# Kernel optimization log

Measured on AMD Instinct MI355X. Metric: run time of the kernel, lower is better.

The kernel has to match this reference:

```python
import jax, jax.numpy as jnp
import numpy as np

N_NODES = 50000
N_EDGES = 800000
IN_F = 256
HID = 128
OUT_F = 128
HEADS = 4
NEG_SLOPE = 0.2


def setup_inputs() -> dict:
    key = jax.random.key(0)
    ks = jax.random.split(key, 10)
    x = jax.random.normal(ks[0], (N_NODES, IN_F), dtype=jnp.float32)
    edge_index = jax.random.randint(ks[1], (2, N_EDGES), 0, N_NODES, dtype=jnp.int64)
    # layer 1: in=256 -> heads=4, ch=128
    W1 = jax.random.normal(ks[2], (HEADS * HID, IN_F), dtype=jnp.float32) / np.sqrt(IN_F)
    att_src1 = jax.random.normal(ks[3], (HEADS, HID), dtype=jnp.float32) / np.sqrt(HID)
    att_dst1 = jax.random.normal(ks[4], (HEADS, HID), dtype=jnp.float32) / np.sqrt(HID)
    b1 = jnp.zeros((HID,), dtype=jnp.float32)
    # layer 2: in=128 -> heads=4, ch=128
    W2 = jax.random.normal(ks[5], (HEADS * OUT_F, HID), dtype=jnp.float32) / np.sqrt(HID)
    att_src2 = jax.random.normal(ks[6], (HEADS, OUT_F), dtype=jnp.float32) / np.sqrt(OUT_F)
    att_dst2 = jax.random.normal(ks[7], (HEADS, OUT_F), dtype=jnp.float32) / np.sqrt(OUT_F)
    b2 = jnp.zeros((OUT_F,), dtype=jnp.float32)
    return {"x": x, "edge_index": edge_index,
            "W1": W1, "att_src1": att_src1, "att_dst1": att_dst1, "b1": b1,
            "W2": W2, "att_src2": att_src2, "att_dst2": att_dst2, "b2": b2}


def gat_conv(x, src, dst, W, att_src, att_dst, b, heads, ch):
    n = x.shape[0]
    xh = (x @ W.T).reshape(n, heads, ch)                 # [N,H,C]
    a_s = jnp.einsum('nhc,hc->nh', xh, att_src)          # [N,H]
    a_d = jnp.einsum('nhc,hc->nh', xh, att_dst)
    alpha = a_s[src] + a_d[dst]                          # [E,H]
    alpha = jnp.where(alpha >= 0, alpha, NEG_SLOPE * alpha)
    # segment softmax over destination nodes
    amax = jax.ops.segment_max(alpha, dst, num_segments=n)
    amax = jnp.where(jnp.isfinite(amax), amax, 0.0)
    e = jnp.exp(alpha - amax[dst])                       # [E,H]
    denom = jax.ops.segment_sum(e, dst, num_segments=n)  # [N,H]
    coef = e / (denom[dst] + 1e-16)                      # [E,H]
    msg = xh[src] * coef[:, :, None]                     # [E,H,C]
    out = jax.ops.segment_sum(msg, dst, num_segments=n)  # [N,H,C]
    return out.mean(axis=1) + b                          # concat=False -> mean over heads


def reference(x, edge_index, W1, att_src1, att_dst1, b1, W2, att_src2, att_dst2, b2):
    n = x.shape[0]
    loops = jnp.arange(n, dtype=edge_index.dtype)
    src = jnp.concatenate([edge_index[0], loops])        # add_self_loops=True (PyG default)
    dst = jnp.concatenate([edge_index[1], loops])
    h = gat_conv(x, src, dst, W1, att_src1, att_dst1, b1, HEADS, HID)
    return gat_conv(h, src, dst, W2, att_src2, att_dst2, b2, HEADS, OUT_F)
```

## Files before the change

### kernel.cpp

```cpp
#include <hip/hip_runtime.h>
#include <hip/hip_fp16.h>
#include <math.h>

#define N_NODES 50000
#define MPAD    50176
#define N_EDGES 800000
#define E_TOT   (N_EDGES + N_NODES)
#define EB      ((E_TOT + 255) / 256)
#define HEADS   4
#define NEG_SLOPE 0.2f
#define SBLK    ((N_NODES + 255) / 256)

typedef unsigned int u32;
typedef unsigned short u16;
typedef __attribute__((ext_vector_type(8))) _Float16 f16x8;
typedef __attribute__((ext_vector_type(4))) float f32x4;



__global__ __launch_bounds__(256) void prep(const int* __restrict__ ei,
                                            int* __restrict__ deg,
                                            int* __restrict__ epos,
                                            const float* __restrict__ W1,
                                            __half* __restrict__ B1,
                                            const float* __restrict__ W2,
                                            __half* __restrict__ B2,
                                            const float* __restrict__ att_s1,
                                            const float* __restrict__ att_d1,
                                            const float* __restrict__ att_s2,
                                            const float* __restrict__ att_d2,
                                            float* __restrict__ ws1,
                                            float* __restrict__ wd1,
                                            float* __restrict__ ws2,
                                            float* __restrict__ wd2) {
  int b = blockIdx.x, tid = threadIdx.x;
  if (b < EB) {
    int e = b * 256 + tid;
    if (e < E_TOT) {
      int dst = (e < N_EDGES) ? ei[N_EDGES + e] : (e - N_EDGES);
      epos[e] = atomicAdd(&deg[dst], 1);
    }
    return;
  }
  if (b < EB + 128) {
    int k4 = (b - EB) * 256 + tid;
    float4 v = ((const float4*)W1)[k4];
    __half2 h01 = __float22half2_rn(make_float2(v.x, v.y));
    __half2 h23 = __float22half2_rn(make_float2(v.z, v.w));
    uint2 pk = make_uint2(*(u32*)&h01, *(u32*)&h23);
    int r = k4 >> 6, h = r >> 7, j = r & 127;
    ((uint2*)B1)[j * 256 + h * 64 + (k4 & 63)] = pk;
    return;
  }
  if (b < EB + 192) {
    int k4 = (b - EB - 128) * 256 + tid;
    float4 v = ((const float4*)W2)[k4];
    __half2 h01 = __float22half2_rn(make_float2(v.x, v.y));
    __half2 h23 = __float22half2_rn(make_float2(v.z, v.w));
    uint2 pk = make_uint2(*(u32*)&h01, *(u32*)&h23);
    int r = k4 >> 5, h = r >> 7, j = r & 127;
    ((uint2*)B2)[j * 128 + h * 32 + (k4 & 31)] = pk;
    return;
  }
  int bw = b - (EB + 192);
  int h = bw & 3;
  if (bw < 8) {
    const float* att = (bw < 4) ? att_s1 : att_d1;
    float* o = (bw < 4) ? ws1 : wd1;
    int k = tid;
    float acc = 0.f;
    for (int c = 0; c < 128; ++c)
      acc = fmaf(att[h * 128 + c], W1[(size_t)(h * 128 + c) * 256 + k], acc);
    o[h * 256 + k] = acc;
  } else {
    const float* att = (bw < 12) ? att_s2 : att_d2;
    float* o = (bw < 12) ? ws2 : wd2;
    if (tid < 128) {
      int k = tid;
      float acc = 0.f;
      for (int c = 0; c < 128; ++c)
        acc = fmaf(att[h * 128 + c], W2[(size_t)(h * 128 + c) * 128 + k], acc);
      o[h * 128 + k] = acc;
    }
  }
}


__global__ __launch_bounds__(256) void scan_blocks(const int* __restrict__ deg,
                                                   int* __restrict__ row_ptr,
                                                   int* __restrict__ bsum) {
  __shared__ int sh[256];
  int tid = threadIdx.x;
  int idx = blockIdx.x * 256 + tid;
  int v = (idx < N_NODES) ? deg[idx] : 0;
  sh[tid] = v;
  __syncthreads();
#pragma unroll
  for (int off = 1; off < 256; off <<= 1) {
    int t = (tid >= off) ? sh[tid - off] : 0;
    __syncthreads();
    sh[tid] += t;
    __syncthreads();
  }
  if (idx < N_NODES) row_ptr[idx + 1] = sh[tid];
  if (tid == 255) bsum[blockIdx.x] = sh[255];
}

__global__ __launch_bounds__(256) void scan_tops(int* __restrict__ bsum) {
  __shared__ int sh[256];
  int tid = threadIdx.x;
  int v = (tid < SBLK) ? bsum[tid] : 0;
  sh[tid] = v;
  __syncthreads();
#pragma unroll
  for (int off = 1; off < 256; off <<= 1) {
    int t = (tid >= off) ? sh[tid - off] : 0;
    __syncthreads();
    sh[tid] += t;
    __syncthreads();
  }
  if (tid < SBLK) bsum[tid] = sh[tid] - v;
}

__global__ __launch_bounds__(256) void scan_add(const int* __restrict__ bsum,
                                                int* __restrict__ row_ptr) {
  int idx = blockIdx.x * 256 + threadIdx.x;
  int off = bsum[blockIdx.x];
  if (idx < N_NODES) row_ptr[idx + 1] += off;
  if (idx == 0) row_ptr[0] = 0;
}

__device__ __forceinline__ float leaky_exp(float a) {
  a = (a >= 0.f) ? a : NEG_SLOPE * a;
  return __expf(a);
}


__global__ __launch_bounds__(256) void scatter_pos(const int* __restrict__ ei,
                                                   const int* __restrict__ epos,
                                                   const int* __restrict__ row_ptr,
                                                   int2* __restrict__ col2) {
  int e = blockIdx.x * 256 + threadIdx.x;
  if (e >= E_TOT) return;
  int src, dst;
  if (e < N_EDGES) { src = ei[e]; dst = ei[N_EDGES + e]; }
  else             { src = e - N_EDGES; dst = src; }
  int slot = row_ptr[dst] + epos[e];
  col2[slot] = make_int2(src, dst);
}


__global__ __launch_bounds__(256) void edge_weights(const int2* __restrict__ col2,
                                                    const float* __restrict__ as_,
                                                    const float* __restrict__ ad_,
                                                    float4* __restrict__ wtab) {
  int i = blockIdx.x * 256 + threadIdx.x;
  if (i >= E_TOT) return;
  int2 sd = col2[i];
  float4 a = ((const float4*)as_)[sd.x];
  float4 d = ((const float4*)ad_)[sd.y];
  float4 w;
  w.x = leaky_exp(a.x + d.x);
  w.y = leaky_exp(a.y + d.y);
  w.z = leaky_exp(a.z + d.z);
  w.w = leaky_exp(a.w + d.w);
  wtab[i] = w;
}


__global__ __launch_bounds__(256) void prep_x(const float* __restrict__ x,
                                              const float* __restrict__ ws1,
                                              const float* __restrict__ wd1,
                                              __half* __restrict__ x16,
                                              float* __restrict__ as_,
                                              float* __restrict__ ad_) {
  int node = (blockIdx.x * 256 + threadIdx.x) >> 6;
  if (node >= N_NODES) return;
  int lane = threadIdx.x & 63;
  int c4 = lane * 4;
  f32x4 xv = *(const f32x4*)(x + (size_t)node * 256 + c4);
  __half2 h01 = __float22half2_rn(make_float2(xv[0], xv[1]));
  __half2 h23 = __float22half2_rn(make_float2(xv[2], xv[3]));
  uint2 pk = make_uint2(*(u32*)&h01, *(u32*)&h23);
  *(uint2*)(x16 + (size_t)node * 256 + c4) = pk;
  float p[8];
#pragma unroll
  for (int v = 0; v < 4; ++v) {
    f32x4 w = *(const f32x4*)(ws1 + v * 256 + c4);
    p[v] = xv[0] * w[0] + xv[1] * w[1] + xv[2] * w[2] + xv[3] * w[3];
    f32x4 u = *(const f32x4*)(wd1 + v * 256 + c4);
    p[4 + v] = xv[0] * u[0] + xv[1] * u[1] + xv[2] * u[2] + xv[3] * u[3];
  }
#pragma unroll
  for (int k = 0; k < 8; ++k)
#pragma unroll
    for (int m = 1; m < 64; m <<= 1)
      p[k] += __shfl_xor(p[k], m, 64);
  if (lane == 0) {
    *(float4*)(as_ + (size_t)node * 4) = make_float4(p[0], p[1], p[2], p[3]);
    *(float4*)(ad_ + (size_t)node * 4) = make_float4(p[4], p[5], p[6], p[7]);
  }
}


__global__ __launch_bounds__(256) void score2(const __half* __restrict__ hrow,
                                              const float* __restrict__ ws2,
                                              const float* __restrict__ wd2,
                                              float* __restrict__ as_,
                                              float* __restrict__ ad_) {
  int node = (blockIdx.x * 256 + threadIdx.x) >> 6;
  if (node >= N_NODES) return;
  int lane = threadIdx.x & 63, c = lane * 2;
  float2 f = __half22float2(*(const __half2*)(hrow + (size_t)node * 128 + c));
  float p[8];
#pragma unroll
  for (int v = 0; v < 4; ++v) {
    float2 w = *(const float2*)(ws2 + v * 128 + c);
    p[v] = f.x * w.x + f.y * w.y;
    float2 u = *(const float2*)(wd2 + v * 128 + c);
    p[4 + v] = f.x * u.x + f.y * u.y;
  }
#pragma unroll
  for (int k = 0; k < 8; ++k)
#pragma unroll
    for (int m = 1; m < 64; m <<= 1)
      p[k] += __shfl_xor(p[k], m, 64);
  if (lane == 0) {
    *(float4*)(as_ + (size_t)node * 4) = make_float4(p[0], p[1], p[2], p[3]);
    *(float4*)(ad_ + (size_t)node * 4) = make_float4(p[4], p[5], p[6], p[7]);
  }
}


template <int CPL>
__global__ __launch_bounds__(256) void gat_aggregate_w(
    const __half* __restrict__ tbl, const float4* __restrict__ wtab,
    const int* __restrict__ row_ptr, const int2* __restrict__ col2,
    __half* __restrict__ agg) {
  constexpr int CHIN = CPL * 64;
  const int* colx = (const int*)col2;
  int node = (blockIdx.x * 256 + threadIdx.x) >> 6;
  if (node >= N_NODES) return;
  int lane = threadIdx.x & 63, cb = lane * CPL;
  const __half* tb = tbl + cb;
  int s = __builtin_amdgcn_readfirstlane(row_ptr[node]);
  int e = __builtin_amdgcn_readfirstlane(row_ptr[node + 1]);

  float acc[4][CPL];
#pragma unroll
  for (int h = 0; h < 4; ++h)
#pragma unroll
    for (int c = 0; c < CPL; ++c) acc[h][c] = 0.f;
  float den[4] = {0.f, 0.f, 0.f, 0.f};

  auto accum = [&](uint2 q, float4 w) {
    float wv[4] = {w.x, w.y, w.z, w.w};
#pragma unroll
    for (int h = 0; h < 4; ++h) den[h] += wv[h];
    float f[CPL];
    float2 f0 = __half22float2(*(__half2*)&q.x);
    f[0] = f0.x; f[1] = f0.y;
    if (CPL == 4) {
      float2 f1 = __half22float2(*(__half2*)&q.y);
      f[2] = f1.x; f[3] = f1.y;
    }
#pragma unroll
    for (int h = 0; h < 4; ++h)
#pragma unroll
      for (int c = 0; c < CPL; ++c)
        acc[h][c] = fmaf(wv[h], f[c], acc[h][c]);
  };
  auto loadq = [&](int src) -> uint2 {
    if (CPL == 4) return *(const uint2*)(tb + (size_t)src * CHIN);
    uint2 r; r.x = *(const u32*)(tb + (size_t)src * CHIN); r.y = 0;
    return r;
  };

  int i = s;
  for (; i + 4 <= e; i += 4) {
    int s0 = __builtin_amdgcn_readfirstlane(colx[2 * i]);
    int s1 = __builtin_amdgcn_readfirstlane(colx[2 * i + 2]);
    int s2 = __builtin_amdgcn_readfirstlane(colx[2 * i + 4]);
    int s3 = __builtin_amdgcn_readfirstlane(colx[2 * i + 6]);
    float4 w0 = wtab[i],     w1 = wtab[i + 1];
    float4 w2 = wtab[i + 2], w3 = wtab[i + 3];
    uint2 q0 = loadq(s0), q1 = loadq(s1), q2 = loadq(s2), q3 = loadq(s3);
    accum(q0, w0); accum(q1, w1); accum(q2, w2); accum(q3, w3);
  }
  for (; i < e; ++i) {
    int s0 = __builtin_amdgcn_readfirstlane(colx[2 * i]);
    float4 w0 = wtab[i];
    accum(loadq(s0), w0);
  }

#pragma unroll
  for (int h = 0; h < 4; ++h) {
    float inv = 1.f / (den[h] + 1e-16f);
    if (CPL == 4) {
      __half2 o0 = __float22half2_rn(make_float2(acc[h][0] * inv, acc[h][1] * inv));
      __half2 o1 = __float22half2_rn(make_float2(acc[h][2] * inv, acc[h][3] * inv));
      *(uint2*)(agg + (size_t)node * 4 * CHIN + h * CHIN + cb) =
          make_uint2(*(u32*)&o0, *(u32*)&o1);
    } else {
      __half2 o0 = __float22half2_rn(make_float2(acc[h][0] * inv, acc[h][1] * inv));
      *(u32*)(agg + (size_t)node * 4 * CHIN + h * CHIN + cb) = *(u32*)&o0;
    }
  }
}


#define GLD16(gp, lp)                                                          \
  __builtin_amdgcn_global_load_lds(                                            \
      (const __attribute__((address_space(1))) u32*)(gp),                      \
      (__attribute__((address_space(3))) u32*)(lp), 16, 0, 0)

template <int K, bool HALF_OUT>
__global__ __launch_bounds__(512, 4) void gemm_mean(
    const __half* __restrict__ A, const __half* __restrict__ Bm,
    const float* __restrict__ bias, void* __restrict__ outv) {
  __shared__ u16 sA[256 * 32];
  __shared__ u16 sB[128 * 32];
  const int tid = threadIdx.x, lane = tid & 63, wave = tid >> 6;
  const int m0 = blockIdx.x * 256;
  const int wm = (wave >> 1) * 64, wn = (wave & 1) * 64;
  const int t = lane & 15, quad = lane >> 4;

  f32x4 acc[4][4];
#pragma unroll
  for (int i = 0; i < 4; i++)
#pragma unroll
    for (int j = 0; j < 4; j++) acc[i][j] = (f32x4){0.f, 0.f, 0.f, 0.f};

  const char* gpA[2]; u32 offA[2];
#pragma unroll
  for (int r = 0; r < 2; ++r) {
    int c = tid + r * 512;
    int row = c >> 2, w16 = c & 3;
    gpA[r] = (const char*)A + ((size_t)(m0 + row) * K) * 2 + w16 * 16;
    offA[r] = (u32)c * 16;
  }
  const char* gpB;
  {
    int row = tid >> 2, w16 = tid & 3;
    gpB = (const char*)Bm + ((size_t)row * K) * 2 + w16 * 16;
  }
  u32 offB = (u32)tid * 16;

  for (int k0 = 0; k0 < K; k0 += 32) {
    __syncthreads();
#pragma unroll
    for (int r = 0; r < 2; ++r) { GLD16(gpA[r], (char*)sA + offA[r]); gpA[r] += 64; }
    GLD16(gpB, (char*)sB + offB); gpB += 64;
    __syncthreads();

    f16x8 a[4], b[4];
#pragma unroll
    for (int i = 0; i < 4; ++i) {
      a[i] = *(const f16x8*)&sA[(wm + t + i * 16) * 32 + quad * 8];
      b[i] = *(const f16x8*)&sB[(wn + t + i * 16) * 32 + quad * 8];
    }
#pragma unroll
    for (int i = 0; i < 4; ++i)
#pragma unroll
      for (int j = 0; j < 4; ++j)
        acc[i][j] = __builtin_amdgcn_mfma_f32_16x16x32_f16(a[i], b[j], acc[i][j], 0, 0, 0);
  }

  float bv[4];
#pragma unroll
  for (int j = 0; j < 4; ++j) bv[j] = bias[wn + j * 16 + t];
#pragma unroll
  for (int i = 0; i < 4; ++i)
#pragma unroll
    for (int j = 0; j < 4; ++j)
#pragma unroll
      for (int r = 0; r < 4; ++r) {
        int m = m0 + wm + i * 16 + quad * 4 + r;
        if (m < N_NODES) {
          int n = wn + j * 16 + t;
          float v = 0.25f * acc[i][j][r] + bv[j];
          if (HALF_OUT) ((__half*)outv)[(size_t)m * 128 + n] = __float2half(v);
          else          ((float*)outv)[(size_t)m * 128 + n] = v;
        }
      }
}


extern "C" void kernel_launch(void* const* d_in, const int* in_sizes, int n_in,
                              void* d_out, int out_size, void* d_ws, size_t ws_size,
                              hipStream_t stream) {
  const float* x      = (const float*)d_in[0];
  const int*   ei     = (const int*)  d_in[1];
  const float* W1     = (const float*)d_in[2];
  const float* att_s1 = (const float*)d_in[3];
  const float* att_d1 = (const float*)d_in[4];
  const float* b1     = (const float*)d_in[5];
  const float* W2     = (const float*)d_in[6];
  const float* att_s2 = (const float*)d_in[7];
  const float* att_d2 = (const float*)d_in[8];
  const float* b2     = (const float*)d_in[9];
  float* out = (float*)d_out;

  char* ws = (char*)d_ws;
  size_t off = 0;
  auto alloc = [&](size_t bytes) -> void* {
    void* p = ws + off;
    off += (bytes + 255) & ~(size_t)255;
    return p;
  };
  __half* x16  = (__half*)alloc((size_t)MPAD * 256 * 2);
  __half* agg1 = (__half*)alloc((size_t)MPAD * 1024 * 2);
  __half* B1p  = (__half*)alloc((size_t)128 * 1024 * 2);
  __half* B2p  = (__half*)alloc((size_t)128 * 512 * 2);
  float* ws1 = (float*)alloc(4 * 256 * 4);
  float* wd1 = (float*)alloc(4 * 256 * 4);
  float* ws2 = (float*)alloc(4 * 128 * 4);
  float* wd2 = (float*)alloc(4 * 128 * 4);
  float* as1 = (float*)alloc((size_t)N_NODES * 4 * 4);
  float* ad1 = (float*)alloc((size_t)N_NODES * 4 * 4);
  float* as2 = (float*)alloc((size_t)N_NODES * 4 * 4);
  float* ad2 = (float*)alloc((size_t)N_NODES * 4 * 4);
  int*   row_ptr = (int*)alloc((size_t)(N_NODES + 1) * 4);
  int*   deg     = (int*)alloc((size_t)N_NODES * 4);
  int*   bsum    = (int*)alloc((size_t)256 * 4);
  int*   epos    = (int*)alloc((size_t)E_TOT * 4);
  int2*  col2    = (int2*)alloc((size_t)E_TOT * 8);
  float4* wtab   = (float4*)alloc((size_t)E_TOT * 16);

  __half* out1 = x16;
  __half* agg2 = agg1;

  const int edge_blocks = (E_TOT + 255) / 256;
  const int node_wave_blocks = (N_NODES + 3) / 4;

  hipMemsetAsync(deg, 0, (size_t)N_NODES * 4, stream);
  prep<<<EB + 208, 256, 0, stream>>>(ei, deg, epos, W1, B1p, W2, B2p,
                                     att_s1, att_d1, att_s2, att_d2,
                                     ws1, wd1, ws2, wd2);
  scan_blocks<<<SBLK, 256, 0, stream>>>(deg, row_ptr, bsum);
  scan_tops<<<1, 256, 0, stream>>>(bsum);
  scan_add<<<SBLK, 256, 0, stream>>>(bsum, row_ptr);
  scatter_pos<<<edge_blocks, 256, 0, stream>>>(ei, epos, row_ptr, col2);

  prep_x<<<node_wave_blocks, 256, 0, stream>>>(x, ws1, wd1, x16, as1, ad1);
  edge_weights<<<edge_blocks, 256, 0, stream>>>(col2, as1, ad1, wtab);
  gat_aggregate_w<4><<<node_wave_blocks, 256, 0, stream>>>(
      x16, wtab, row_ptr, col2, agg1);
  gemm_mean<1024, true><<<MPAD / 256, 512, 0, stream>>>(agg1, B1p, b1, out1);

  score2<<<node_wave_blocks, 256, 0, stream>>>(out1, ws2, wd2, as2, ad2);
  edge_weights<<<edge_blocks, 256, 0, stream>>>(col2, as2, ad2, wtab);
  gat_aggregate_w<2><<<node_wave_blocks, 256, 0, stream>>>(
      out1, wtab, row_ptr, col2, agg2);
  gemm_mean<512, false><<<MPAD / 256, 512, 0, stream>>>(agg2, B2p, b2, out);
}
```

Before: 406.6 us.

## Fuse neighbor aggregation with head-mean projection GEMM via shared memory

Each block now aggregates 16 destination nodes (4 per wave) into an LDS tile of weighted per-head features, then does the projection with MFMA straight from LDS and writes the biased head-mean output. This removes the large intermediate agg buffer (N×1024 halves for layer 1) and its global write and read, plus the separate GEMM launches. In exchange, B is reloaded from global/L2 by every block, each wave handles several nodes one after another, and the GEMM tile is small (16 rows), so MFMA efficiency and load balance may drop.

```diff
diff --git a/kernel.cpp b/kernel.cpp
--- a/kernel.cpp
+++ b/kernel.cpp
@@ -3,13 +3,13 @@
 #include <math.h>
 
 #define N_NODES 50000
-#define MPAD    50176
 #define N_EDGES 800000
 #define E_TOT   (N_EDGES + N_NODES)
 #define EB      ((E_TOT + 255) / 256)
 #define HEADS   4
 #define NEG_SLOPE 0.2f
 #define SBLK    ((N_NODES + 255) / 256)
+#define FBLK    (N_NODES / 16)
 
 typedef unsigned int u32;
 typedef unsigned short u16;
@@ -232,157 +232,120 @@
 }
 
 
-template <int CPL>
-__global__ __launch_bounds__(256) void gat_aggregate_w(
+template <int CPL, bool HALF_OUT>
+__global__ __launch_bounds__(256) void gat_fused(
     const __half* __restrict__ tbl, const float4* __restrict__ wtab,
     const int* __restrict__ row_ptr, const int2* __restrict__ col2,
-    __half* __restrict__ agg) {
+    const __half* __restrict__ Bm, const float* __restrict__ bias,
+    void* __restrict__ outv) {
   constexpr int CHIN = CPL * 64;
+  constexpr int K = 4 * CHIN;
+  constexpr int RST = K + 8;
+  __shared__ u16 sA[16 * RST];
+  const int tid = threadIdx.x, lane = tid & 63, wave = tid >> 6;
+  const int base = blockIdx.x * 16;
+  const int cb = lane * CPL;
+  const __half* tb = tbl + cb;
   const int* colx = (const int*)col2;
-  int node = (blockIdx.x * 256 + threadIdx.x) >> 6;
-  if (node >= N_NODES) return;
-  int lane = threadIdx.x & 63, cb = lane * CPL;
-  const __half* tb = tbl + cb;
-  int s = __builtin_amdgcn_readfirstlane(row_ptr[node]);
-  int e = __builtin_amdgcn_readfirstlane(row_ptr[node + 1]);
-
-  float acc[4][CPL];
-#pragma unroll
-  for (int h = 0; h < 4; ++h)
-#pragma unroll
-    for (int c = 0; c < CPL; ++c) acc[h][c] = 0.f;
-  float den[4] = {0.f, 0.f, 0.f, 0.f};
-
-  auto accum = [&](uint2 q, float4 w) {
-    float wv[4] = {w.x, w.y, w.z, w.w};
-#pragma unroll
-    for (int h = 0; h < 4; ++h) den[h] += wv[h];
-    float f[CPL];
-    float2 f0 = __half22float2(*(__half2*)&q.x);
-    f[0] = f0.x; f[1] = f0.y;
-    if (CPL == 4) {
-      float2 f1 = __half22float2(*(__half2*)&q.y);
-      f[2] = f1.x; f[3] = f1.y;
-    }
+
+  for (int nn = 0; nn < 4; ++nn) {
+    const int row = wave * 4 + nn;
+    const int node = base + row;
+    int s = __builtin_amdgcn_readfirstlane(row_ptr[node]);
+    int e = __builtin_amdgcn_readfirstlane(row_ptr[node + 1]);
+
+    float acc[4][CPL];
 #pragma unroll
     for (int h = 0; h < 4; ++h)
 #pragma unroll
-      for (int c = 0; c < CPL; ++c)
-        acc[h][c] = fmaf(wv[h], f[c], acc[h][c]);
-  };
-  auto loadq = [&](int src) -> uint2 {
-    if (CPL == 4) return *(const uint2*)(tb + (size_t)src * CHIN);
-    uint2 r; r.x = *(const u32*)(tb + (size_t)src * CHIN); r.y = 0;
-    return r;
-  };
-
-  int i = s;
-  for (; i + 4 <= e; i += 4) {
-    int s0 = __builtin_amdgcn_readfirstlane(colx[2 * i]);
-    int s1 = __builtin_amdgcn_readfirstlane(colx[2 * i + 2]);
-    int s2 = __builtin_amdgcn_readfirstlane(colx[2 * i + 4]);
-    int s3 = __builtin_amdgcn_readfirstlane(colx[2 * i + 6]);
-    float4 w0 = wtab[i],     w1 = wtab[i + 1];
-    float4 w2 = wtab[i + 2], w3 = wtab[i + 3];
-    uint2 q0 = loadq(s0), q1 = loadq(s1), q2 = loadq(s2), q3 = loadq(s3);
-    accum(q0, w0); accum(q1, w1); accum(q2, w2); accum(q3, w3);
-  }
-  for (; i < e; ++i) {
-    int s0 = __builtin_amdgcn_readfirstlane(colx[2 * i]);
-    float4 w0 = wtab[i];
-    accum(loadq(s0), w0);
-  }
-
-#pragma unroll
-  for (int h = 0; h < 4; ++h) {
-    float inv = 1.f / (den[h] + 1e-16f);
-    if (CPL == 4) {
-      __half2 o0 = __float22half2_rn(make_float2(acc[h][0] * inv, acc[h][1] * inv));
-      __half2 o1 = __float22half2_rn(make_float2(acc[h][2] * inv, acc[h][3] * inv));
-      *(uint2*)(agg + (size_t)node * 4 * CHIN + h * CHIN + cb) =
-          make_uint2(*(u32*)&o0, *(u32*)&o1);
+      for (int c = 0; c < CPL; ++c) acc[h][c] = 0.f;
+    float den[4] = {0.f, 0.f, 0.f, 0.f};
+
+    auto accum = [&](uint2 q, float4 w) {
+      float wv[4] = {w.x, w.y, w.z, w.w};
+#pragma unroll
+      for (int h = 0; h < 4; ++h) den[h] += wv[h];
+      float f[CPL];
+      float2 f0 = __half22float2(*(__half2*)&q.x);
+      f[0] = f0.x; f[1] = f0.y;
+      if (CPL == 4) {
+        float2 f1 = __half22float2(*(__half2*)&q.y);
+        f[2] = f1.x; f[3] = f1.y;
+      }
+#pragma unroll
+      for (int h = 0; h < 4; ++h)
+#pragma unroll
+        for (int c = 0; c < CPL; ++c)
+          acc[h][c] = fmaf(wv[h], f[c], acc[h][c]);
+    };
+    auto loadq = [&](int src) -> uint2 {
+      if (CPL == 4) return *(const uint2*)(tb + (size_t)src * CHIN);
+      uint2 r; r.x = *(const u32*)(tb + (size_t)src * CHIN); r.y = 0;
+      return r;
+    };
+
+    int i = s;
+    for (; i + 4 <= e; i += 4) {
+      int s0 = __builtin_amdgcn_readfirstlane(colx[2 * i]);
+      int s1 = __builtin_amdgcn_readfirstlane(colx[2 * i + 2]);
+      int s2 = __builtin_amdgcn_readfirstlane(colx[2 * i + 4]);
+      int s3 = __builtin_amdgcn_readfirstlane(colx[2 * i + 6]);
+      float4 w0 = wtab[i],     w1 = wtab[i + 1];
+      float4 w2 = wtab[i + 2], w3 = wtab[i + 3];
+      uint2 q0 = loadq(s0), q1 = loadq(s1), q2 = loadq(s2), q3 = loadq(s3);
+      accum(q0, w0); accum(q1, w1); accum(q2, w2); accum(q3, w3);
+    }
+    for (; i < e; ++i) {
+      int s0 = __builtin_amdgcn_readfirstlane(colx[2 * i]);
+      float4 w0 = wtab[i];
+      accum(loadq(s0), w0);
+    }
+
+#pragma unroll
+    for (int h = 0; h < 4; ++h) {
+      float inv = 1.f / (den[h] + 1e-16f);
+      if (CPL == 4) {
+        __half2 o0 = __float22half2_rn(make_float2(acc[h][0] * inv, acc[h][1] * inv));
+        __half2 o1 = __float22half2_rn(make_float2(acc[h][2] * inv, acc[h][3] * inv));
+        *(uint2*)&sA[row * RST + h * CHIN + cb] = make_uint2(*(u32*)&o0, *(u32*)&o1);
+      } else {
+        __half2 o0 = __float22half2_rn(make_float2(acc[h][0] * inv, acc[h][1] * inv));
+        *(u32*)&sA[row * RST + h * CHIN + cb] = *(u32*)&o0;
+      }
+    }
+  }
+  __syncthreads();
+
+  const int t = lane & 15, quad = lane >> 4;
+  f32x4 acc0 = (f32x4){0.f, 0.f, 0.f, 0.f};
+  f32x4 acc1 = (f32x4){0.f, 0.f, 0.f, 0.f};
+  const char* gB0 = (const char*)Bm + ((size_t)(wave * 32 + t) * K + quad * 8) * 2;
+  const char* gB1 = gB0 + (size_t)16 * K * 2;
+#pragma unroll 4
+  for (int k0 = 0; k0 < K; k0 += 32) {
+    f16x8 b0 = *(const f16x8*)(gB0 + (size_t)k0 * 2);
+    f16x8 b1 = *(const f16x8*)(gB1 + (size_t)k0 * 2);
+    f16x8 a = *(const f16x8*)&sA[t * RST + k0 + quad * 8];
+    acc0 = __builtin_amdgcn_mfma_f32_16x16x32_f16(a, b0, acc0, 0, 0, 0);
+    acc1 = __builtin_amdgcn_mfma_f32_16x16x32_f16(a, b1, acc1, 0, 0, 0);
+  }
+
+  const int n0 = wave * 32 + t;
+  const float bv0 = bias[n0], bv1 = bias[n0 + 16];
+#pragma unroll
+  for (int r = 0; r < 4; ++r) {
+    int m = quad * 4 + r;
+    int node = base + m;
+    float v0 = 0.25f * acc0[r] + bv0;
+    float v1 = 0.25f * acc1[r] + bv1;
+    if (HALF_OUT) {
+      ((__half*)outv)[(size_t)node * 128 + n0]      = __float2half(v0);
+      ((__half*)outv)[(size_t)node * 128 + n0 + 16] = __float2half(v1);
     } else {
-      __half2 o0 = __float22half2_rn(make_float2(acc[h][0] * inv, acc[h][1] * inv));
-      *(u32*)(agg + (size_t)node * 4 * CHIN + h * CHIN + cb) = *(u32*)&o0;
-    }
-  }
-}
-
-
-#define GLD16(gp, lp)                                                          \
-  __builtin_amdgcn_global_load_lds(                                            \
-      (const __attribute__((address_space(1))) u32*)(gp),                      \
-      (__attribute__((address_space(3))) u32*)(lp), 16, 0, 0)
-
-template <int K, bool HALF_OUT>
-__global__ __launch_bounds__(512, 4) void gemm_mean(
-    const __half* __restrict__ A, const __half* __restrict__ Bm,
-    const float* __restrict__ bias, void* __restrict__ outv) {
-  __shared__ u16 sA[256 * 32];
-  __shared__ u16 sB[128 * 32];
-  const int tid = threadIdx.x, lane = tid & 63, wave = tid >> 6;
-  const int m0 = blockIdx.x * 256;
-  const int wm = (wave >> 1) * 64, wn = (wave & 1) * 64;
-  const int t = lane & 15, quad = lane >> 4;
-
-  f32x4 acc[4][4];
-#pragma unroll
-  for (int i = 0; i < 4; i++)
-#pragma unroll
-    for (int j = 0; j < 4; j++) acc[i][j] = (f32x4){0.f, 0.f, 0.f, 0.f};
-
-  const char* gpA[2]; u32 offA[2];
-#pragma unroll
-  for (int r = 0; r < 2; ++r) {
-    int c = tid + r * 512;
-    int row = c >> 2, w16 = c & 3;
-    gpA[r] = (const char*)A + ((size_t)(m0 + row) * K) * 2 + w16 * 16;
-    offA[r] = (u32)c * 16;
-  }
-  const char* gpB;
-  {
-    int row = tid >> 2, w16 = tid & 3;
-    gpB = (const char*)Bm + ((size_t)row * K) * 2 + w16 * 16;
-  }
-  u32 offB = (u32)tid * 16;
-
-  for (int k0 = 0; k0 < K; k0 += 32) {
-    __syncthreads();
-#pragma unroll
-    for (int r = 0; r < 2; ++r) { GLD16(gpA[r], (char*)sA + offA[r]); gpA[r] += 64; }
-    GLD16(gpB, (char*)sB + offB); gpB += 64;
-    __syncthreads();
-
-    f16x8 a[4], b[4];
-#pragma unroll
-    for (int i = 0; i < 4; ++i) {
-      a[i] = *(const f16x8*)&sA[(wm + t + i * 16) * 32 + quad * 8];
-      b[i] = *(const f16x8*)&sB[(wn + t + i * 16) * 32 + quad * 8];
-    }
-#pragma unroll
-    for (int i = 0; i < 4; ++i)
-#pragma unroll
-      for (int j = 0; j < 4; ++j)
-        acc[i][j] = __builtin_amdgcn_mfma_f32_16x16x32_f16(a[i], b[j], acc[i][j], 0, 0, 0);
-  }
-
-  float bv[4];
-#pragma unroll
-  for (int j = 0; j < 4; ++j) bv[j] = bias[wn + j * 16 + t];
-#pragma unroll
-  for (int i = 0; i < 4; ++i)
-#pragma unroll
-    for (int j = 0; j < 4; ++j)
-#pragma unroll
-      for (int r = 0; r < 4; ++r) {
-        int m = m0 + wm + i * 16 + quad * 4 + r;
-        if (m < N_NODES) {
-          int n = wn + j * 16 + t;
-          float v = 0.25f * acc[i][j][r] + bv[j];
-          if (HALF_OUT) ((__half*)outv)[(size_t)m * 128 + n] = __float2half(v);
-          else          ((float*)outv)[(size_t)m * 128 + n] = v;
-        }
-      }
+      ((float*)outv)[(size_t)node * 128 + n0]      = v0;
+      ((float*)outv)[(size_t)node * 128 + n0 + 16] = v1;
+    }
+  }
 }
 
 
@@ -408,8 +371,8 @@
     off += (bytes + 255) & ~(size_t)255;
     return p;
   };
-  __half* x16  = (__half*)alloc((size_t)MPAD * 256 * 2);
-  __half* agg1 = (__half*)alloc((size_t)MPAD * 1024 * 2);
+  __half* x16  = (__half*)alloc((size_t)N_NODES * 256 * 2);
+  __half* out1 = (__half*)alloc((size_t)N_NODES * 128 * 2);
   __half* B1p  = (__half*)alloc((size_t)128 * 1024 * 2);
   __half* B2p  = (__half*)alloc((size_t)128 * 512 * 2);
   float* ws1 = (float*)alloc(4 * 256 * 4);
@@ -427,9 +390,6 @@
   int2*  col2    = (int2*)alloc((size_t)E_TOT * 8);
   float4* wtab   = (float4*)alloc((size_t)E_TOT * 16);
 
-  __half* out1 = x16;
-  __half* agg2 = agg1;
-
   const int edge_blocks = (E_TOT + 255) / 256;
   const int node_wave_blocks = (N_NODES + 3) / 4;
 
@@ -444,13 +404,11 @@
 
   prep_x<<<node_wave_blocks, 256, 0, stream>>>(x, ws1, wd1, x16, as1, ad1);
   edge_weights<<<edge_blocks, 256, 0, stream>>>(col2, as1, ad1, wtab);
-  gat_aggregate_w<4><<<node_wave_blocks, 256, 0, stream>>>(
-      x16, wtab, row_ptr, col2, agg1);
-  gemm_mean<1024, true><<<MPAD / 256, 512, 0, stream>>>(agg1, B1p, b1, out1);
+  gat_fused<4, true><<<FBLK, 256, 0, stream>>>(x16, wtab, row_ptr, col2,
+                                               B1p, b1, out1);
 
   score2<<<node_wave_blocks, 256, 0, stream>>>(out1, ws2, wd2, as2, ad2);
   edge_weights<<<edge_blocks, 256, 0, stream>>>(col2, as2, ad2, wtab);
-  gat_aggregate_w<2><<<node_wave_blocks, 256, 0, stream>>>(
-      out1, wtab, row_ptr, col2, agg2);
-  gemm_mean<512, false><<<MPAD / 256, 512, 0, stream>>>(agg2, B2p, b2, out);
-}
+  gat_fused<2, false><<<FBLK, 256, 0, stream>>>(out1, wtab, row_ptr, col2,
+                                                B2p, b2, out);
+}
```

Measured after the change: 448.0 us. +10.2%, slower.
